# Performance work log

Measured on AMD Instinct MI355X. Metric: run time of the kernel, lower is better.

The kernel has to match this reference:

```python
import jax, jax.numpy as jnp
import numpy as np

# Fixed average-trace buffer from the module (length 120)
AVG = jnp.asarray([0.0256,0.0823,0.1157,0.1315,0.1366,0.1369,0.1347,0.1308,0.1259,0.1205,0.1146,0.1086,0.1028,0.097,0.0913,0.0858,0.0805,0.0756,0.0708,0.0664,0.0623,0.0584,0.0549,0.0515,0.0485,0.0456,0.0429,0.0404,0.0381,0.036,0.034,0.0321,0.0304,0.0287,0.0272,0.0258,0.0245,0.0233,0.0222,0.0211,0.0201,0.0191,0.0182,0.0173,0.0165,0.0158,0.015,0.0143,0.0137,0.013,0.0125,0.0119,0.0114,0.0108,0.0104,0.0099,0.0095,0.0091,0.0087,0.0083,0.008,0.0077,0.0074,0.0071,0.0068,0.0065,0.0062,0.006,0.0058,0.0055,0.0053,0.005,0.0049,0.0047,0.0045,0.0044,0.0042,0.004,0.0039,0.0038,0.0036,0.0034,0.0033,0.0032,0.0031,0.003,0.0029,0.0028,0.0027,0.0026,0.0025,0.0024,0.0023,0.0022,0.0021,0.0021,0.002,0.0019,0.0018,0.0018,0.0017,0.0017,0.0016,0.0016,0.0015,0.0015,0.0014,0.0014,0.0013,0.0013,0.0013,0.0012,0.0012,0.0011,0.0011,0.0011,0.001,0.001,0.001,0.0009], dtype=jnp.float32)


def _lstm(x, w_ih, w_hh, b):
    """PyTorch-semantics single-layer LSTM. x: [N,T,D], w_ih: [4H,D], w_hh: [4H,H], b: [4H] (= b_ih + b_hh). Gate order i,f,g,o."""
    xp = jnp.einsum('ntd,gd->ntg', x, w_ih) + b  # precompute input projections: [N,T,4H]
    N = x.shape[0]
    H = w_hh.shape[1]
    h0 = jnp.zeros((N, H), x.dtype)

    def step(carry, xt):
        h, c = carry
        g = xt + h @ w_hh.T  # [N,4H]
        i, f, gg, o = jnp.split(g, 4, axis=-1)
        c = jax.nn.sigmoid(f) * c + jax.nn.sigmoid(i) * jnp.tanh(gg)
        h = jax.nn.sigmoid(o) * jnp.tanh(c)
        return (h, c), h

    _, hs = jax.lax.scan(step, (h0, h0), jnp.swapaxes(xp, 0, 1))  # hs: [T,N,H]
    return jnp.swapaxes(hs, 0, 1)  # [N,T,H]


def setup_inputs() -> dict:
    key = jax.random.key(0)
    ks = jax.random.split(key, 7)
    N, F, H = 32768, 12, 30
    s1 = 1.0 / float(np.sqrt(H))  # torch LSTM init: U(-1/sqrt(H), 1/sqrt(H))
    s2 = 1.0                      # second LSTM hidden=1 -> scale 1
    return {
        'features': jax.random.normal(ks[0], (N, F), jnp.float32),
        'w_ih1': jax.random.uniform(ks[1], (4 * H, F + 1), jnp.float32, -s1, s1),
        'w_hh1': jax.random.uniform(ks[2], (4 * H, H), jnp.float32, -s1, s1),
        'b1': jax.random.uniform(ks[3], (4 * H,), jnp.float32, -s1, s1),
        'w_ih2': jax.random.uniform(ks[4], (4, H), jnp.float32, -s2, s2),
        'w_hh2': jax.random.uniform(ks[5], (4, 1), jnp.float32, -s2, s2),
        'b2': jax.random.uniform(ks[6], (4,), jnp.float32, -s2, s2),
    }


def reference(features, w_ih1, w_hh1, b1, w_ih2, w_hh2, b2):
    N, F = features.shape
    T = AVG.shape[0]  # 120
    x = jnp.broadcast_to(features[:, None, :], (N, T, F))          # repeat features over time
    trace = jnp.broadcast_to(AVG[None, :, None], (N, T, 1))        # average trace channel
    x = jnp.concatenate([x, trace], axis=2)                        # [N,120,13]
    h1 = _lstm(x, w_ih1, w_hh1, b1)                                # [N,120,30]
    return _lstm(h1, w_ih2, w_hh2, b2)                             # [N,120,1]
```

## Files before the change

kernel.cpp:

```cpp
#include <hip/hip_runtime.h>

typedef __attribute__((ext_vector_type(8))) short bf16x8;
typedef __attribute__((ext_vector_type(4))) float f32x4;

__device__ __constant__ float AVG_D[120] = {
    0.0256f,0.0823f,0.1157f,0.1315f,0.1366f,0.1369f,0.1347f,0.1308f,0.1259f,0.1205f,
    0.1146f,0.1086f,0.1028f,0.0970f,0.0913f,0.0858f,0.0805f,0.0756f,0.0708f,0.0664f,
    0.0623f,0.0584f,0.0549f,0.0515f,0.0485f,0.0456f,0.0429f,0.0404f,0.0381f,0.0360f,
    0.0340f,0.0321f,0.0304f,0.0287f,0.0272f,0.0258f,0.0245f,0.0233f,0.0222f,0.0211f,
    0.0201f,0.0191f,0.0182f,0.0173f,0.0165f,0.0158f,0.0150f,0.0143f,0.0137f,0.0130f,
    0.0125f,0.0119f,0.0114f,0.0108f,0.0104f,0.0099f,0.0095f,0.0091f,0.0087f,0.0083f,
    0.0080f,0.0077f,0.0074f,0.0071f,0.0068f,0.0065f,0.0062f,0.0060f,0.0058f,0.0055f,
    0.0053f,0.0050f,0.0049f,0.0047f,0.0045f,0.0044f,0.0042f,0.0040f,0.0039f,0.0038f,
    0.0036f,0.0034f,0.0033f,0.0032f,0.0031f,0.0030f,0.0029f,0.0028f,0.0027f,0.0026f,
    0.0025f,0.0024f,0.0023f,0.0022f,0.0021f,0.0021f,0.0020f,0.0019f,0.0018f,0.0018f,
    0.0017f,0.0017f,0.0016f,0.0016f,0.0015f,0.0015f,0.0014f,0.0014f,0.0013f,0.0013f,
    0.0013f,0.0012f,0.0012f,0.0011f,0.0011f,0.0011f,0.0010f,0.0010f,0.0010f,0.0009f
};

__device__ __forceinline__ float sigf(float x) {
    return __builtin_amdgcn_rcpf(1.0f + __expf(-x));
}
__device__ __forceinline__ float tanh_fast(float x) {
    return fmaf(2.0f, __builtin_amdgcn_rcpf(1.0f + __expf(-2.0f * x)), -1.0f);
}
__device__ __forceinline__ unsigned short tb(float x) {
    return (unsigned short)(__float_as_uint(x) >> 16);
}
__device__ __forceinline__ float fb(unsigned short h) {
    return __uint_as_float(((unsigned)h) << 16);
}

__global__ void pack_weights(const float* __restrict__ w_ih1,
                             const float* __restrict__ w_hh1,
                             const float* __restrict__ b1,
                             const float* __restrict__ w_ih2,
                             const float* __restrict__ b2,
                             float* __restrict__ ws) {
    unsigned short* whi = (unsigned short*)ws;
    unsigned short* wlo = (unsigned short*)(ws + 2048);
    float* bconst = ws + 4096;
    float* wih1f  = ws + 4224;
    const int tid = threadIdx.x;
    for (int idx = tid; idx < 4096; idx += 256) {
        const int T = idx >> 9, lane = (idx >> 3) & 63, j = idx & 7;
        const int r = 16 * T + (lane & 15);
        const int k = ((lane >> 4) & 3) * 8 + j;
        const int u = r >> 2, q = r & 3;
        float v = 0.0f;
        if (u < 30) {
            if (k < 30)       v = w_hh1[(q * 30 + u) * 30 + k];
            else if (k == 30) v = w_ih1[(q * 30 + u) * 13 + 12];
        } else if (u == 30 && k < 30) {
            v = w_ih2[q * 30 + k];
        }
        const unsigned short hi = tb(v);
        whi[idx] = hi;
        wlo[idx] = tb(v - fb(hi));
    }
    for (int r = tid; r < 128; r += 256) {
        const int u = r >> 2, q = r & 3;
        bconst[r] = (u < 30) ? b1[q * 30 + u] : ((u == 30) ? b2[q] : 0.0f);
    }
    for (int idx = tid; idx < 1536; idx += 256) {
        const int r = idx / 12, d = idx % 12;
        const int u = r >> 2, q = r & 3;
        wih1f[idx] = (u < 30) ? w_ih1[(q * 30 + u) * 13 + d] : 0.0f;
    }
}

__global__ __launch_bounds__(256, 2)
void lstm_mfma_kernel(const float* __restrict__ feat,
                      const float* __restrict__ w_hh2,
                      const float* __restrict__ ws,
                      float* __restrict__ out) {
    __shared__ float hx_s[4][32 * 17];
    __shared__ __align__(16) float out_s[64 * 124];

    const int tid  = threadIdx.x;
    const int lane = tid & 63;
    const int wv   = tid >> 6;
    const int s    = lane & 15;
    const int quad = lane >> 4;
    const int seq  = (blockIdx.x * 4 + wv) * 16 + s;
    float* hx = &hx_s[wv][0];

    for (int i = lane; i < 544; i += 64) hx[i] = 0.0f;

    bf16x8 Ahi[8], Alo[8];
    {
        const unsigned short* whi = (const unsigned short*)ws;
        const unsigned short* wlo = (const unsigned short*)(ws + 2048);
#pragma unroll
        for (int T = 0; T < 8; T++) {
            Ahi[T] = *(const bf16x8*)(whi + T * 512 + lane * 8);
            Alo[T] = *(const bf16x8*)(wlo + T * 512 + lane * 8);
        }
    }

    float f0[12];
    {
        const float4* fp = reinterpret_cast<const float4*>(feat + seq * 12);
        float4 A = fp[0], B = fp[1], C = fp[2];
        f0[0]=A.x; f0[1]=A.y; f0[2]=A.z; f0[3]=A.w;
        f0[4]=B.x; f0[5]=B.y; f0[6]=B.z; f0[7]=B.w;
        f0[8]=C.x; f0[9]=C.y; f0[10]=C.z; f0[11]=C.w;
    }
    f32x4 projb[8];
    {
        const float* bconst = ws + 4096;
        const float* wih1f  = ws + 4224;
#pragma unroll
        for (int T = 0; T < 8; T++) {
#pragma unroll
            for (int g = 0; g < 4; g++) {
                const int r = 16 * T + 4 * quad + g;
                float acc = bconst[r];
#pragma unroll
                for (int d = 0; d < 12; d++) acc = fmaf(f0[d], wih1f[r * 12 + d], acc);
                projb[T][g] = acc;
            }
        }
    }

    float c1[8];
#pragma unroll
    for (int T = 0; T < 8; T++) c1[T] = 0.0f;
    float h2 = 0.0f, c2 = 0.0f;
    const float wh20 = w_hh2[0], wh21 = w_hh2[1], wh22 = w_hh2[2], wh23 = w_hh2[3];

#pragma unroll 1
    for (int t = 0; t <= 120; t++) {
        bf16x8 Bhi, Blo;
#pragma unroll
        for (int j = 0; j < 8; j++) {
            const int u = 8 * quad + j;
            const float hv = hx[u * 17 + s];
            const unsigned short hh = tb(hv);
            Bhi[j] = (short)hh;
            Blo[j] = (short)tb(hv - fb(hh));
        }
        if (quad == 3) {
            const float at = (t < 120) ? AVG_D[t] : 0.0f;
            const unsigned short ah = tb(at);
            Bhi[6] = (short)ah;
            Blo[6] = (short)tb(at - fb(ah));
        }

        f32x4 D[8];
#pragma unroll
        for (int T = 0; T < 8; T++)
            D[T] = __builtin_amdgcn_mfma_f32_16x16x32_bf16(Alo[T], Bhi, projb[T], 0, 0, 0);
#pragma unroll
        for (int T = 0; T < 8; T++)
            D[T] = __builtin_amdgcn_mfma_f32_16x16x32_bf16(Ahi[T], Blo, D[T], 0, 0, 0);
#pragma unroll
        for (int T = 0; T < 8; T++)
            D[T] = __builtin_amdgcn_mfma_f32_16x16x32_bf16(Ahi[T], Bhi, D[T], 0, 0, 0);

        if (t >= 1 && quad == 2) {
            const float g0 = D[7][0] + h2 * wh20;
            const float g1 = D[7][1] + h2 * wh21;
            const float g2 = D[7][2] + h2 * wh22;
            const float g3 = D[7][3] + h2 * wh23;
            c2 = sigf(g1) * c2 + sigf(g0) * tanh_fast(g2);
            h2 = sigf(g3) * tanh_fast(c2);
            out_s[(wv * 16 + s) * 124 + (t - 1)] = h2;
        }

        if (t < 120) {
#pragma unroll
            for (int T = 0; T < 7; T++) {
                const float ci = sigf(D[T][0]);
                const float cf = sigf(D[T][1]);
                const float cg = tanh_fast(D[T][2]);
                const float co = sigf(D[T][3]);
                const float ck = cf * c1[T] + ci * cg;
                c1[T] = ck;
                hx[(4 * T + quad) * 17 + s] = co * tanh_fast(ck);
            }
            if (quad < 2) {
                const float ci = sigf(D[7][0]);
                const float cf = sigf(D[7][1]);
                const float cg = tanh_fast(D[7][2]);
                const float co = sigf(D[7][3]);
                const float ck = cf * c1[7] + ci * cg;
                c1[7] = ck;
                hx[(28 + quad) * 17 + s] = co * tanh_fast(ck);
            }
        }
    }

    __syncthreads();
    float* outb = out + (size_t)blockIdx.x * 64 * 120;
#pragma unroll
    for (int it = 0; it < 8; it++) {
        const int fi = it * 256 + tid;
        if (fi < 1920) {
            const int sq = fi / 30, j = fi % 30;
            const float4 v = *reinterpret_cast<const float4*>(&out_s[sq * 124 + j * 4]);
            *reinterpret_cast<float4*>(&outb[sq * 120 + j * 4]) = v;
        }
    }
}

extern "C" void kernel_launch(void* const* d_in, const int* in_sizes, int n_in,
                              void* d_out, int out_size, void* d_ws, size_t ws_size,
                              hipStream_t stream) {
    (void)in_sizes; (void)n_in; (void)out_size; (void)ws_size;
    const float* feat  = (const float*)d_in[0];
    const float* w_ih1 = (const float*)d_in[1];
    const float* w_hh1 = (const float*)d_in[2];
    const float* b1    = (const float*)d_in[3];
    const float* w_ih2 = (const float*)d_in[4];
    const float* w_hh2 = (const float*)d_in[5];
    const float* b2    = (const float*)d_in[6];
    float* ws  = (float*)d_ws;
    float* out = (float*)d_out;

    hipLaunchKernelGGL(pack_weights, dim3(1), dim3(256), 0, stream,
                       w_ih1, w_hh1, b1, w_ih2, b2, ws);
    hipLaunchKernelGGL(lstm_mfma_kernel, dim3(512), dim3(256), 0, stream,
                       feat, w_hh2, ws, out);
}
```

Before: 285.0 us.

## Split LSTM gate tiles across two waves per sequence group with double-buffered LDS

Each 16-sequence group is now handled by a 128-thread block whose two waves each compute half of the gate MFMA tiles and activations. The hidden state is exchanged through a double-buffered shared array with a block barrier per timestep. This shortens the per-wave serial chain per step and doubles the wave count, to expose more parallelism on a latency-bound recurrence. It adds a barrier each step and duplicates the B-operand conversion in both waves.

Result: no change. 286.6 us (+0.6%).

```diff
diff --git a/kernel.cpp b/kernel.cpp
--- a/kernel.cpp
+++ b/kernel.cpp
@@ -69,32 +69,31 @@
     }
 }
 
-__global__ __launch_bounds__(256, 2)
+__global__ __launch_bounds__(128, 4)
 void lstm_mfma_kernel(const float* __restrict__ feat,
                       const float* __restrict__ w_hh2,
                       const float* __restrict__ ws,
                       float* __restrict__ out) {
-    __shared__ float hx_s[4][32 * 17];
-    __shared__ __align__(16) float out_s[64 * 124];
+    __shared__ float hx[2][32 * 17];
+    __shared__ __align__(16) float out_s[16 * 124];
 
     const int tid  = threadIdx.x;
     const int lane = tid & 63;
-    const int wv   = tid >> 6;
+    const int wr   = __builtin_amdgcn_readfirstlane(tid >> 6);
     const int s    = lane & 15;
     const int quad = lane >> 4;
-    const int seq  = (blockIdx.x * 4 + wv) * 16 + s;
-    float* hx = &hx_s[wv][0];
-
-    for (int i = lane; i < 544; i += 64) hx[i] = 0.0f;
-
-    bf16x8 Ahi[8], Alo[8];
+    const int seq  = blockIdx.x * 16 + s;
+
+    for (int i = tid; i < 1088; i += 128) (&hx[0][0])[i] = 0.0f;
+
+    bf16x8 Ahi[4], Alo[4];
     {
         const unsigned short* whi = (const unsigned short*)ws;
         const unsigned short* wlo = (const unsigned short*)(ws + 2048);
 #pragma unroll
-        for (int T = 0; T < 8; T++) {
-            Ahi[T] = *(const bf16x8*)(whi + T * 512 + lane * 8);
-            Alo[T] = *(const bf16x8*)(wlo + T * 512 + lane * 8);
+        for (int Tl = 0; Tl < 4; Tl++) {
+            Ahi[Tl] = *(const bf16x8*)(whi + (4 * wr + Tl) * 512 + lane * 8);
+            Alo[Tl] = *(const bf16x8*)(wlo + (4 * wr + Tl) * 512 + lane * 8);
         }
     }
 
@@ -106,36 +105,41 @@
         f0[4]=B.x; f0[5]=B.y; f0[6]=B.z; f0[7]=B.w;
         f0[8]=C.x; f0[9]=C.y; f0[10]=C.z; f0[11]=C.w;
     }
-    f32x4 projb[8];
+    f32x4 projb[4];
     {
         const float* bconst = ws + 4096;
         const float* wih1f  = ws + 4224;
 #pragma unroll
-        for (int T = 0; T < 8; T++) {
+        for (int Tl = 0; Tl < 4; Tl++) {
 #pragma unroll
             for (int g = 0; g < 4; g++) {
-                const int r = 16 * T + 4 * quad + g;
+                const int r = 64 * wr + 16 * Tl + 4 * quad + g;
                 float acc = bconst[r];
 #pragma unroll
                 for (int d = 0; d < 12; d++) acc = fmaf(f0[d], wih1f[r * 12 + d], acc);
-                projb[T][g] = acc;
+                projb[Tl][g] = acc;
             }
         }
     }
 
-    float c1[8];
-#pragma unroll
-    for (int T = 0; T < 8; T++) c1[T] = 0.0f;
+    float c1[4];
+#pragma unroll
+    for (int Tl = 0; Tl < 4; Tl++) c1[Tl] = 0.0f;
     float h2 = 0.0f, c2 = 0.0f;
     const float wh20 = w_hh2[0], wh21 = w_hh2[1], wh22 = w_hh2[2], wh23 = w_hh2[3];
 
+    __syncthreads();
+
 #pragma unroll 1
     for (int t = 0; t <= 120; t++) {
+        const float* hb = hx[t & 1];
+        float*       hn = hx[(t & 1) ^ 1];
+
         bf16x8 Bhi, Blo;
 #pragma unroll
         for (int j = 0; j < 8; j++) {
             const int u = 8 * quad + j;
-            const float hv = hx[u * 17 + s];
+            const float hv = hb[u * 17 + s];
             const unsigned short hh = tb(hv);
             Bhi[j] = (short)hh;
             Blo[j] = (short)tb(hv - fb(hh));
@@ -147,56 +151,51 @@
             Blo[6] = (short)tb(at - fb(ah));
         }
 
-        f32x4 D[8];
-#pragma unroll
-        for (int T = 0; T < 8; T++)
-            D[T] = __builtin_amdgcn_mfma_f32_16x16x32_bf16(Alo[T], Bhi, projb[T], 0, 0, 0);
-#pragma unroll
-        for (int T = 0; T < 8; T++)
-            D[T] = __builtin_amdgcn_mfma_f32_16x16x32_bf16(Ahi[T], Blo, D[T], 0, 0, 0);
-#pragma unroll
-        for (int T = 0; T < 8; T++)
-            D[T] = __builtin_amdgcn_mfma_f32_16x16x32_bf16(Ahi[T], Bhi, D[T], 0, 0, 0);
-
-        if (t >= 1 && quad == 2) {
-            const float g0 = D[7][0] + h2 * wh20;
-            const float g1 = D[7][1] + h2 * wh21;
-            const float g2 = D[7][2] + h2 * wh22;
-            const float g3 = D[7][3] + h2 * wh23;
+        f32x4 D[4];
+#pragma unroll
+        for (int Tl = 0; Tl < 4; Tl++)
+            D[Tl] = __builtin_amdgcn_mfma_f32_16x16x32_bf16(Alo[Tl], Bhi, projb[Tl], 0, 0, 0);
+#pragma unroll
+        for (int Tl = 0; Tl < 4; Tl++)
+            D[Tl] = __builtin_amdgcn_mfma_f32_16x16x32_bf16(Ahi[Tl], Blo, D[Tl], 0, 0, 0);
+#pragma unroll
+        for (int Tl = 0; Tl < 4; Tl++)
+            D[Tl] = __builtin_amdgcn_mfma_f32_16x16x32_bf16(Ahi[Tl], Bhi, D[Tl], 0, 0, 0);
+
+        if (t >= 1 && wr == 1 && quad == 2) {
+            const float g0 = D[3][0] + h2 * wh20;
+            const float g1 = D[3][1] + h2 * wh21;
+            const float g2 = D[3][2] + h2 * wh22;
+            const float g3 = D[3][3] + h2 * wh23;
             c2 = sigf(g1) * c2 + sigf(g0) * tanh_fast(g2);
             h2 = sigf(g3) * tanh_fast(c2);
-            out_s[(wv * 16 + s) * 124 + (t - 1)] = h2;
+            out_s[s * 124 + (t - 1)] = h2;
         }
 
         if (t < 120) {
 #pragma unroll
-            for (int T = 0; T < 7; T++) {
-                const float ci = sigf(D[T][0]);
-                const float cf = sigf(D[T][1]);
-                const float cg = tanh_fast(D[T][2]);
-                const float co = sigf(D[T][3]);
-                const float ck = cf * c1[T] + ci * cg;
-                c1[T] = ck;
-                hx[(4 * T + quad) * 17 + s] = co * tanh_fast(ck);
+            for (int Tl = 0; Tl < 4; Tl++) {
+                const int u = 16 * wr + 4 * Tl + quad;
+                if (u < 30) {
+                    const float ci = sigf(D[Tl][0]);
+                    const float cf = sigf(D[Tl][1]);
+                    const float cg = tanh_fast(D[Tl][2]);
+                    const float co = sigf(D[Tl][3]);
+                    const float ck = cf * c1[Tl] + ci * cg;
+                    c1[Tl] = ck;
+                    hn[u * 17 + s] = co * tanh_fast(ck);
+                }
             }
-            if (quad < 2) {
-                const float ci = sigf(D[7][0]);
-                const float cf = sigf(D[7][1]);
-                const float cg = tanh_fast(D[7][2]);
-                const float co = sigf(D[7][3]);
-                const float ck = cf * c1[7] + ci * cg;
-                c1[7] = ck;
-                hx[(28 + quad) * 17 + s] = co * tanh_fast(ck);
-            }
-        }
-    }
-
-    __syncthreads();
-    float* outb = out + (size_t)blockIdx.x * 64 * 120;
-#pragma unroll
-    for (int it = 0; it < 8; it++) {
-        const int fi = it * 256 + tid;
-        if (fi < 1920) {
+        }
+
+        __syncthreads();
+    }
+
+    float* outb = out + (size_t)blockIdx.x * 16 * 120;
+#pragma unroll
+    for (int it = 0; it < 4; it++) {
+        const int fi = it * 128 + tid;
+        if (fi < 480) {
             const int sq = fi / 30, j = fi % 30;
             const float4 v = *reinterpret_cast<const float4*>(&out_s[sq * 124 + j * 4]);
             *reinterpret_cast<float4*>(&outb[sq * 120 + j * 4]) = v;
@@ -220,6 +219,6 @@
 
     hipLaunchKernelGGL(pack_weights, dim3(1), dim3(256), 0, stream,
                        w_ih1, w_hh1, b1, w_ih2, b2, ws);
-    hipLaunchKernelGGL(lstm_mfma_kernel, dim3(512), dim3(256), 0, stream,
+    hipLaunchKernelGGL(lstm_mfma_kernel, dim3(2048), dim3(128), 0, stream,
                        feat, w_hh2, ws, out);
 }
```
